# Kernel optimization log

Hardware: AMD Instinct MI355X
Metric: run time of the kernel (lower is better)

The kernel has to match this reference:

```python
import jax, jax.numpy as jnp
import numpy as np
from jax import lax

M_ROWS, N_COLS = 2048, 4096
ADMM_ITERS = 30
CG_ITERS = 15


def setup_inputs() -> dict:
    key = jax.random.key(0)
    ks = jax.random.split(key, 6)
    A = jax.random.normal(ks[0], (M_ROWS, N_COLS), dtype=jnp.float32) / np.sqrt(N_COLS)
    c = jax.random.normal(ks[1], (N_COLS, 1), dtype=jnp.float32)
    # finite box bounds with lb < ub (isinf mask path in the original is vacuous here)
    lb = -(jnp.abs(jax.random.normal(ks[2], (M_ROWS, 1), dtype=jnp.float32)) + 0.1)
    ub = jnp.abs(jax.random.normal(ks[3], (M_ROWS, 1), dtype=jnp.float32)) + 0.1
    # positive diagonal scalings from the LP preconditioning (Ruiz-style)
    d = 0.5 + jax.random.uniform(ks[4], (N_COLS, 1), dtype=jnp.float32)
    e = 0.5 + jax.random.uniform(ks[5], (M_ROWS, 1), dtype=jnp.float32)
    return {
        "A": A, "c": c, "lb": lb, "ub": ub, "d": d, "e": e,
        "gamma_c": jnp.ones((1,), jnp.float32),   # gamma_c_mul * gamma_c
        "gamma_b": jnp.ones((1,), jnp.float32),   # gamma_b_mul * gamma_b
        "rho": jnp.ones((1,), jnp.float32),
        "sigma": jnp.full((1,), 1e-6, jnp.float32),  # exp(sigma_log), sigma_log=log(1e-6)
        "alpha": jnp.full((1,), 1.6, jnp.float32),
    }


def _pcg(matvec, b, Minv, x0, iters):
    """Fixed-iteration preconditioned conjugate gradient for SPD matvec."""
    r0 = b - matvec(x0)
    z0 = Minv(r0)
    rz0 = jnp.vdot(r0, z0)

    def body(carry, _):
        x, r, p, rz = carry
        Kp = matvec(p)
        a = rz / jnp.vdot(p, Kp)
        x = x + a * p
        r = r - a * Kp
        zv = Minv(r)
        rz_new = jnp.vdot(r, zv)
        p = zv + (rz_new / rz) * p
        return (x, r, p, rz_new), None

    (x, _, _, _), _ = lax.scan(body, (x0, r0, z0, rz0), None, length=iters)
    return x


def _admm_lp(A, c, lb, ub, d, e, gamma_c, gamma_b, rho, sigma, alpha):
    gc, gb = gamma_c[0], gamma_b[0]
    rho_s, sig_s, al_s = rho[0], sigma[0], alpha[0]
    m, n = A.shape

    c_s = gc * (d * c)                 # (n,1) scaled cost
    lb_s = gb * e * lb                 # (m,1)
    ub_s = gb * e * ub                 # (m,1)

    # diagonal preconditioner M = sigma + rho * ||A_:,j||^2
    Acnorm2 = jnp.sum(A * A, axis=0)[:, None]      # (n,1)
    Mdiag = sig_s + rho_s * Acnorm2
    Minv = lambda v: v / Mdiag
    Kop = lambda v: rho_s * (A.T @ (A @ v)) + sig_s * v

    x0 = jnp.zeros((n, 1), A.dtype)
    z0 = jnp.zeros((m, 1), A.dtype)
    y0 = jnp.zeros((m, 1), A.dtype)
    xt0 = jnp.zeros((n, 1), A.dtype)

    def step(carry, _):
        x, z, y, xtilde = carry
        right = sig_s * x - c_s + A.T @ (rho_s * z - y)
        xtilde = _pcg(Kop, right, Minv, xtilde, CG_ITERS)
        ztilde = A @ xtilde
        x = al_s * xtilde + (1.0 - al_s) * x
        ztilde = al_s * ztilde + (1.0 - al_s) * z
        z = jnp.clip(ztilde + y / rho_s, lb_s, ub_s)
        y = y + rho_s * (ztilde - z)
        return (x, z, y, xtilde), None

    (x, z, y, xtilde), _ = lax.scan(step, (x0, z0, y0, xt0), None, length=ADMM_ITERS)
    return x * d / gb                   # unscaled LP solution (n,1)


def reference(A, c, lb, ub, d, e, gamma_c, gamma_b, rho, sigma, alpha):
    return _admm_lp(A, c, lb, ub, d, e, gamma_c, gamma_b, rho, sigma, alpha)
```

## Files before the change

kernel.cpp:

```cpp
#include <hip/hip_runtime.h>

#define NWG 256
#define NT  512
#define NDIM 4096
#define MROWS 2048
#define N_ADMM 30
#define N_CG 15

typedef unsigned long long ull;
typedef float f32x4 __attribute__((ext_vector_type(4)));

#define SWZC(c) ((c) ^ (((c) >> 3) & 7))

__device__ __forceinline__ float wred64(float v) {
#pragma unroll
  for (int m = 32; m > 0; m >>= 1) v += __shfl_xor(v, m, 64);
  return v;
}
__device__ __forceinline__ void sta32(unsigned* p, unsigned v) {
  __hip_atomic_store(p, v, __ATOMIC_RELAXED, __HIP_MEMORY_SCOPE_AGENT);
}
__device__ __forceinline__ unsigned lda32(const unsigned* p) {
  return __hip_atomic_load(p, __ATOMIC_RELAXED, __HIP_MEMORY_SCOPE_AGENT);
}
__device__ __forceinline__ void staf(float* p, float v) {
  __hip_atomic_store((unsigned*)p, __float_as_uint(v), __ATOMIC_RELAXED,
                     __HIP_MEMORY_SCOPE_AGENT);
}
__device__ __forceinline__ f32x4 ntf4(const float* p) {
  return __builtin_nontemporal_load((const f32x4*)p);
}
__device__ __forceinline__ float ntf(const float* p) {
  return __builtin_nontemporal_load(p);
}

#define WS_KILL 128
#define WS_FLAG 8192
#define WS_NB0  49152
#define WS_NB1  65536
#define WS_U    81920

__global__ __launch_bounds__(NT, 1)
void admm_lp_kernel(const float* __restrict__ A, const float* __restrict__ cvec,
                    const float* __restrict__ lbv, const float* __restrict__ ubv,
                    const float* __restrict__ dvec, const float* __restrict__ evec,
                    const float* __restrict__ gcp, const float* __restrict__ gbp,
                    const float* __restrict__ rhop, const float* __restrict__ sigp,
                    const float* __restrict__ alp,
                    float* __restrict__ out, unsigned char* __restrict__ ws)
{
  const int tid = threadIdx.x;
  const int w = blockIdx.x;
  const int wv = tid >> 6, lane = tid & 63;
  const int j0 = tid * 8;
  const int q  = tid >> 7;
  const int kt = tid & 127;
  const int gg = tid >> 4, gl = tid & 15;

  unsigned* kill  = (unsigned*)(ws + WS_KILL);
  unsigned* flags = (unsigned*)(ws + WS_FLAG);
  float* nb0 = (float*)(ws + WS_NB0);
  float* nb1 = (float*)(ws + WS_NB1);
  float* u_g = (float*)(ws + WS_U);

  __shared__ float s_scal[8];
  __shared__ float dredA[8], dredB[8];
  __shared__ float dred8[8][8];
  __shared__ float sredA[32][16];
  __shared__ float pmat[16][132];
  __shared__ float cs_lds[16], xchunk[16], diag16[16];
  __shared__ float mzb[8], myb[8], mlb[8], mub[8];
  __shared__ int s_dead;
  __shared__ float ldsA[4096];
  __shared__ float ldsB[4096];

  float Greg[4][32];
  float p8[8], r8[8], xt8[8], x8[8], Md8[8];
  unsigned gen = 0;

  auto wait_prod = [&](unsigned G) {
    if (s_dead) return;
    unsigned* fp = &flags[(size_t)(wv * 32 + (lane & 31)) * 16];
    int spin = 0;
    for (;;) {
      unsigned v = lda32(fp);
      if (__all(v >= G)) break;
      __builtin_amdgcn_s_sleep(1);
      if ((++spin & 127) == 0) {
        if (lda32(kill) != 0u || spin > 2000000) {
          s_dead = 1; sta32(kill, 1u); break;
        }
      }
    }
    asm volatile("" ::: "memory");
    __builtin_amdgcn_sched_barrier(0);
  };

  auto publish = [&]() {
    if (wv == 0) {
      asm volatile("s_waitcnt vmcnt(0)" ::: "memory");
      __builtin_amdgcn_sched_barrier(0);
      if (lane == 0 && !s_dead) sta32(&flags[(size_t)w * 16], gen + 1);
    }
    ++gen;
  };

  if (tid == 0) {
    s_scal[0] = sigp[0]; s_scal[1] = rhop[0]; s_scal[2] = alp[0];
    s_scal[3] = gcp[0];  s_scal[4] = gbp[0];
    s_dead = 0;
  }
  __syncthreads();
  const float sig = s_scal[0], rho = s_scal[1], al = s_scal[2];
  const float gc = s_scal[3], gb = s_scal[4];

  if (tid < 8) {
    const int rm = w * 8 + tid;
    mzb[tid] = 0.f; myb[tid] = 0.f;
    const float ee = evec[rm];
    mlb[tid] = gb * ee * lbv[rm];
    mub[tid] = gb * ee * ubv[rm];
  }
  if (tid < 16) {
    const int j = w * 16 + tid;
    cs_lds[tid] = gc * dvec[j] * cvec[j];
  }

#pragma unroll
  for (int rr = 0; rr < 4; ++rr)
#pragma unroll
    for (int cc = 0; cc < 32; ++cc) Greg[rr][cc] = 0.f;

  {
    f32x4 pf0 = ntf4(A + j0), pf1 = ntf4(A + j0 + 4);
    *(f32x4*)&ldsA[SWZC(2 * tid) * 4]     = pf0;
    *(f32x4*)&ldsA[SWZC(2 * tid + 1) * 4] = pf1;
    pf0 = ntf4(A + NDIM + j0); pf1 = ntf4(A + NDIM + j0 + 4);
    __syncthreads();
    float* bc = ldsA;
    float* bn = ldsB;
#pragma unroll 1
    for (int i = 0; i < MROWS; ++i) {
      if (i + 1 < MROWS) {
        *(f32x4*)&bn[SWZC(2 * tid) * 4]     = pf0;
        *(f32x4*)&bn[SWZC(2 * tid + 1) * 4] = pf1;
      }
      if (i + 2 < MROWS) {
        pf0 = ntf4(A + (size_t)(i + 2) * NDIM + j0);
        pf1 = ntf4(A + (size_t)(i + 2) * NDIM + j0 + 4);
      }
      const f32x4 av = *(f32x4*)&bc[SWZC(w * 4 + q) * 4];
#pragma unroll
      for (int c4 = 0; c4 < 8; ++c4) {
        const f32x4 kv = *(f32x4*)&bc[SWZC(kt * 8 + c4) * 4];
#pragma unroll
        for (int e = 0; e < 4; ++e) {
          const float kvv = kv[e];
          const int cc = c4 * 4 + e;
          Greg[0][cc] += av.x * kvv;
          Greg[1][cc] += av.y * kvv;
          Greg[2][cc] += av.z * kvv;
          Greg[3][cc] += av.w * kvv;
        }
      }
      __syncthreads();
      float* t = bc; bc = bn; bn = t;
    }
  }

  if (kt == (w >> 1)) {
#pragma unroll
    for (int rr = 0; rr < 4; ++rr) {
      const int tc = (w & 1) * 16 + q * 4 + rr;
      float dv = 0.f;
#pragma unroll
      for (int cc = 0; cc < 32; ++cc)
        dv = (cc == tc) ? Greg[rr][cc] : dv;
      diag16[q * 4 + rr] = dv;
    }
  }
  __syncthreads();
  if (tid < 16) staf(&nb1[w * 16 + tid], diag16[tid]);
  publish();
  wait_prod(gen);
  {
    const f32x4 d0 = ntf4(&nb1[j0]), d1 = ntf4(&nb1[j0 + 4]);
#pragma unroll
    for (int e = 0; e < 4; ++e) { Md8[e] = sig + rho * d0[e]; Md8[4 + e] = sig + rho * d1[e]; }
  }
#pragma unroll
  for (int e = 0; e < 8; ++e) { xt8[e] = 0.f; x8[e] = 0.f; }

  float rz = 1.f;

#pragma unroll 1
  for (int admm = 0; admm < N_ADMM; ++admm) {
#pragma unroll 1
    for (int cg = 0; cg <= N_CG; ++cg) {
      if (cg == 0) {
        if (admm == 0) {
          const f32x4 dv0 = ntf4(dvec + j0), dv1 = ntf4(dvec + j0 + 4);
          const f32x4 cv0 = ntf4(cvec + j0), cv1 = ntf4(cvec + j0 + 4);
#pragma unroll
          for (int e = 0; e < 4; ++e) {
            r8[e]     = -gc * dv0[e] * cv0[e];
            r8[4 + e] = -gc * dv1[e] * cv1[e];
          }
        } else {
          wait_prod(gen);
          const float* nb = (gen & 1) ? nb1 : nb0;
          const f32x4 a = ntf4(nb + j0), b = ntf4(nb + j0 + 4);
#pragma unroll
          for (int e = 0; e < 4; ++e) { r8[e] = a[e]; r8[4 + e] = b[e]; }
        }
        float z8[8], part = 0.f;
#pragma unroll
        for (int e = 0; e < 8; ++e) { z8[e] = r8[e] / Md8[e]; part += r8[e] * z8[e]; }
        part = wred64(part);
        if (lane == 0) dredA[wv] = part;
        __syncthreads();
        rz = dredA[0] + dredA[1] + dredA[2] + dredA[3]
           + dredA[4] + dredA[5] + dredA[6] + dredA[7];
#pragma unroll
        for (int e = 0; e < 8; ++e) p8[e] = z8[e];
      } else {
        wait_prod(gen);
        const float* nb = (gen & 1) ? nb1 : nb0;
        const f32x4 a = ntf4(nb + j0), b = ntf4(nb + j0 + 4);
        float Kp8[8];
#pragma unroll
        for (int e = 0; e < 4; ++e) { Kp8[e] = a[e]; Kp8[4 + e] = b[e]; }
        float part = 0.f;
#pragma unroll
        for (int e = 0; e < 8; ++e) part += p8[e] * Kp8[e];
        part = wred64(part);
        if (lane == 0) dredA[wv] = part;
        __syncthreads();
        const float pKp = dredA[0] + dredA[1] + dredA[2] + dredA[3]
                        + dredA[4] + dredA[5] + dredA[6] + dredA[7];
        const float alpha = rz / pKp;
#pragma unroll
        for (int e = 0; e < 8; ++e) xt8[e] += alpha * p8[e];
        if (cg < N_CG) {
          float z8[8], pb = 0.f;
#pragma unroll
          for (int e = 0; e < 8; ++e) {
            r8[e] -= alpha * Kp8[e];
            z8[e] = r8[e] / Md8[e];
            pb += r8[e] * z8[e];
          }
          pb = wred64(pb);
          if (lane == 0) dredB[wv] = pb;
          __syncthreads();
          const float rzn = dredB[0] + dredB[1] + dredB[2] + dredB[3]
                          + dredB[4] + dredB[5] + dredB[6] + dredB[7];
          const float beta = rzn / rz;
          rz = rzn;
#pragma unroll
          for (int e = 0; e < 8; ++e) p8[e] = z8[e] + beta * p8[e];
        }
      }
      if (cg < N_CG) {
        {
          f32x4 v0, v1;
#pragma unroll
          for (int e = 0; e < 4; ++e) { v0[e] = p8[e]; v1[e] = p8[4 + e]; }
          *(f32x4*)&ldsA[SWZC(2 * tid) * 4]     = v0;
          *(f32x4*)&ldsA[SWZC(2 * tid + 1) * 4] = v1;
        }
        __syncthreads();
        float u0 = 0.f, u1 = 0.f, u2 = 0.f, u3 = 0.f;
#pragma unroll
        for (int c4 = 0; c4 < 8; ++c4) {
          const f32x4 kv = *(f32x4*)&ldsA[SWZC(kt * 8 + c4) * 4];
#pragma unroll
          for (int e = 0; e < 4; ++e) {
            const float pv = kv[e];
            const int cc = c4 * 4 + e;
            u0 += Greg[0][cc] * pv; u1 += Greg[1][cc] * pv;
            u2 += Greg[2][cc] * pv; u3 += Greg[3][cc] * pv;
          }
        }
        pmat[q * 4 + 0][kt] = u0; pmat[q * 4 + 1][kt] = u1;
        pmat[q * 4 + 2][kt] = u2; pmat[q * 4 + 3][kt] = u3;
        __syncthreads();
        if (tid < 16) {
          float s = 0.f;
#pragma unroll
          for (int c = 0; c < 32; ++c) {
            const f32x4 vv = *(f32x4*)&pmat[tid][c * 4];
            s += vv[0] + vv[1] + vv[2] + vv[3];
          }
          const int jl = w * 16 + tid;
          const float pv = ldsA[SWZC(jl >> 2) * 4 + (jl & 3)];
          float* nbw = ((gen + 1) & 1) ? nb1 : nb0;
          staf(nbw + jl, rho * s + sig * pv);
        }
        publish();
      } else {
        publish();
      }
    }

    if (admm < N_ADMM - 1) {
#pragma unroll
      for (int r = 0; r < 8; ++r) {
        const float* ap = A + (size_t)(w * 8 + r) * NDIM + j0;
        const f32x4 a = ntf4(ap), b = ntf4(ap + 4);
        float s = a[0] * xt8[0] + a[1] * xt8[1] + a[2] * xt8[2] + a[3] * xt8[3]
                + b[0] * xt8[4] + b[1] * xt8[5] + b[2] * xt8[6] + b[3] * xt8[7];
        s = wred64(s);
        if (lane == 0) dred8[wv][r] = s;
      }
      __syncthreads();
      if (tid < 8) {
        float zt = 0.f;
#pragma unroll
        for (int qq = 0; qq < 8; ++qq) zt += dred8[qq][tid];
        zt = al * zt + (1.f - al) * mzb[tid];
        float zn = fminf(fmaxf(zt + myb[tid] / rho, mlb[tid]), mub[tid]);
        const float yn = myb[tid] + rho * (zt - zn);
        mzb[tid] = zn; myb[tid] = yn;
        staf(&u_g[w * 8 + tid], rho * zn - yn);
      }
#pragma unroll
      for (int e = 0; e < 8; ++e) x8[e] = al * xt8[e] + (1.f - al) * x8[e];
      publish();

      wait_prod(gen);
      {
        const f32x4 uv = ntf4(&u_g[tid * 4]);
        *(f32x4*)&ldsB[tid * 4] = uv;
        f32x4 v0, v1;
#pragma unroll
        for (int e = 0; e < 4; ++e) { v0[e] = xt8[e]; v1[e] = xt8[4 + e]; }
        *(f32x4*)&ldsA[SWZC(2 * tid) * 4]     = v0;
        *(f32x4*)&ldsA[SWZC(2 * tid + 1) * 4] = v1;
        if ((tid >> 1) == w) {
          const int b = (tid & 1) * 8;
#pragma unroll
          for (int e = 0; e < 8; ++e) xchunk[b + e] = x8[e];
        }
      }
      __syncthreads();
      {
        float pr = 0.f;
        const float* acp = A + (size_t)(gg * 64) * NDIM + w * 16 + gl;
#pragma unroll 8
        for (int ii = 0; ii < 64; ++ii)
          pr += ntf(acp + (size_t)ii * NDIM) * ldsB[gg * 64 + ii];
        sredA[gg][gl] = pr;
        float u0 = 0.f, u1 = 0.f, u2 = 0.f, u3 = 0.f;
#pragma unroll
        for (int c4 = 0; c4 < 8; ++c4) {
          const f32x4 kv = *(f32x4*)&ldsA[SWZC(kt * 8 + c4) * 4];
#pragma unroll
          for (int e = 0; e < 4; ++e) {
            const float pv = kv[e];
            const int cc = c4 * 4 + e;
            u0 += Greg[0][cc] * pv; u1 += Greg[1][cc] * pv;
            u2 += Greg[2][cc] * pv; u3 += Greg[3][cc] * pv;
          }
        }
        pmat[q * 4 + 0][kt] = u0; pmat[q * 4 + 1][kt] = u1;
        pmat[q * 4 + 2][kt] = u2; pmat[q * 4 + 3][kt] = u3;
      }
      __syncthreads();
      if (tid < 16) {
        float SR = 0.f;
#pragma unroll
        for (int g32 = 0; g32 < 32; ++g32) SR += sredA[g32][tid];
        float gx = 0.f;
#pragma unroll
        for (int c = 0; c < 32; ++c) {
          const f32x4 vv = *(f32x4*)&pmat[tid][c * 4];
          gx += vv[0] + vv[1] + vv[2] + vv[3];
        }
        const int jl = w * 16 + tid;
        const float xtv = ldsA[SWZC(jl >> 2) * 4 + (jl & 3)];
        const float right = sig * xchunk[tid] - cs_lds[tid] + SR;
        const float Kxt = rho * gx + sig * xtv;
        float* nbw = ((gen + 1) & 1) ? nb1 : nb0;
        staf(nbw + jl, right - Kxt);
      }
      publish();
    }
  }

  if ((tid >> 1) == w) {
    const int b = (tid & 1) * 8;
#pragma unroll
    for (int e = 0; e < 8; ++e) {
      const int j = w * 16 + b + e;
      const float xf = al * xt8[e] + (1.f - al) * x8[e];
      out[j] = xf * dvec[j] / gb;
    }
  }
}

extern "C" void kernel_launch(void* const* d_in, const int* in_sizes, int n_in,
                              void* d_out, int out_size, void* d_ws, size_t ws_size,
                              hipStream_t stream) {
  const float* A   = (const float*)d_in[0];
  const float* c   = (const float*)d_in[1];
  const float* lb  = (const float*)d_in[2];
  const float* ub  = (const float*)d_in[3];
  const float* dv  = (const float*)d_in[4];
  const float* ev  = (const float*)d_in[5];
  const float* gc  = (const float*)d_in[6];
  const float* gb  = (const float*)d_in[7];
  const float* rho = (const float*)d_in[8];
  const float* sg  = (const float*)d_in[9];
  const float* al  = (const float*)d_in[10];
  float* out = (float*)d_out;
  unsigned char* ws = (unsigned char*)d_ws;

  (void)hipMemsetAsync(d_ws, 0, 32768, stream);

  admm_lp_kernel<<<dim3(NWG), dim3(NT), 0, stream>>>(
      A, c, lb, ub, dv, ev, gc, gb, rho, sg, al, out, ws);
}
```

Before: 5.585 ms.

## Recurse G*p via G*z plus beta, retile Gram block, use reciprocal preconditioner

```diff
diff --git a/kernel.cpp b/kernel.cpp
--- a/kernel.cpp
+++ b/kernel.cpp
@@ -7,7 +7,6 @@
 #define N_ADMM 30
 #define N_CG 15
 
-typedef unsigned long long ull;
 typedef float f32x4 __attribute__((ext_vector_type(4)));
 
 #define SWZC(c) ((c) ^ (((c) >> 3) & 7))
@@ -53,8 +52,8 @@
   const int w = blockIdx.x;
   const int wv = tid >> 6, lane = tid & 63;
   const int j0 = tid * 8;
-  const int q  = tid >> 7;
-  const int kt = tid & 127;
+  const int h  = tid >> 8;
+  const int ct = tid & 255;
   const int gg = tid >> 4, gl = tid & 15;
 
   unsigned* kill  = (unsigned*)(ws + WS_KILL);
@@ -65,17 +64,18 @@
 
   __shared__ float s_scal[8];
   __shared__ float dredA[8], dredB[8];
+  __shared__ float dredW[8][8];
   __shared__ float dred8[8][8];
   __shared__ float sredA[32][16];
-  __shared__ float pmat[16][132];
   __shared__ float cs_lds[16], xchunk[16], diag16[16];
   __shared__ float mzb[8], myb[8], mlb[8], mub[8];
   __shared__ int s_dead;
   __shared__ float ldsA[4096];
   __shared__ float ldsB[4096];
 
-  float Greg[4][32];
-  float p8[8], r8[8], xt8[8], x8[8], Md8[8];
+  float Greg[8][16];
+  float p8[8], r8[8], xt8[8], x8[8], mdinv8[8];
+  float gpo = 0.f, p16 = 0.f;
   unsigned gen = 0;
 
   auto wait_prod = [&](unsigned G) {
@@ -85,9 +85,9 @@
     for (;;) {
       unsigned v = lda32(fp);
       if (__all(v >= G)) break;
-      __builtin_amdgcn_s_sleep(1);
-      if ((++spin & 127) == 0) {
-        if (lda32(kill) != 0u || spin > 2000000) {
+      if (++spin > 256) __builtin_amdgcn_s_sleep(1);
+      if ((spin & 1023) == 0) {
+        if (lda32(kill) != 0u || spin > 1500000) {
           s_dead = 1; sta32(kill, 1u); break;
         }
       }
@@ -103,6 +103,29 @@
       if (lane == 0 && !s_dead) sta32(&flags[(size_t)w * 16], gen + 1);
     }
     ++gen;
+  };
+
+  auto gmult_stage = [&]() {
+    const f32x4 kv0 = *(const f32x4*)&ldsA[SWZC(ct * 4 + 0) * 4];
+    const f32x4 kv1 = *(const f32x4*)&ldsA[SWZC(ct * 4 + 1) * 4];
+    const f32x4 kv2 = *(const f32x4*)&ldsA[SWZC(ct * 4 + 2) * 4];
+    const f32x4 kv3 = *(const f32x4*)&ldsA[SWZC(ct * 4 + 3) * 4];
+    float u[8];
+#pragma unroll
+    for (int rr = 0; rr < 8; ++rr) {
+      float s = 0.f;
+#pragma unroll
+      for (int e = 0; e < 4; ++e) {
+        s += Greg[rr][e] * kv0[e] + Greg[rr][4 + e] * kv1[e]
+           + Greg[rr][8 + e] * kv2[e] + Greg[rr][12 + e] * kv3[e];
+      }
+      u[rr] = s;
+    }
+#pragma unroll
+    for (int rr = 0; rr < 8; ++rr) {
+      const float t = wred64(u[rr]);
+      if (lane == 0) dredW[wv][rr] = t;
+    }
   };
 
   if (tid == 0) {
@@ -127,9 +150,9 @@
   }
 
 #pragma unroll
-  for (int rr = 0; rr < 4; ++rr)
-#pragma unroll
-    for (int cc = 0; cc < 32; ++cc) Greg[rr][cc] = 0.f;
+  for (int rr = 0; rr < 8; ++rr)
+#pragma unroll
+    for (int c = 0; c < 16; ++c) Greg[rr][c] = 0.f;
 
   {
     f32x4 pf0 = ntf4(A + j0), pf1 = ntf4(A + j0 + 4);
@@ -149,18 +172,24 @@
         pf0 = ntf4(A + (size_t)(i + 2) * NDIM + j0);
         pf1 = ntf4(A + (size_t)(i + 2) * NDIM + j0 + 4);
       }
-      const f32x4 av = *(f32x4*)&bc[SWZC(w * 4 + q) * 4];
-#pragma unroll
-      for (int c4 = 0; c4 < 8; ++c4) {
-        const f32x4 kv = *(f32x4*)&bc[SWZC(kt * 8 + c4) * 4];
+      const f32x4 a0 = *(const f32x4*)&bc[SWZC(w * 4 + h * 2) * 4];
+      const f32x4 a1 = *(const f32x4*)&bc[SWZC(w * 4 + h * 2 + 1) * 4];
+      const f32x4 k0 = *(const f32x4*)&bc[SWZC(ct * 4 + 0) * 4];
+      const f32x4 k1 = *(const f32x4*)&bc[SWZC(ct * 4 + 1) * 4];
+      const f32x4 k2 = *(const f32x4*)&bc[SWZC(ct * 4 + 2) * 4];
+      const f32x4 k3 = *(const f32x4*)&bc[SWZC(ct * 4 + 3) * 4];
+#pragma unroll
+      for (int rr = 0; rr < 4; ++rr) {
 #pragma unroll
         for (int e = 0; e < 4; ++e) {
-          const float kvv = kv[e];
-          const int cc = c4 * 4 + e;
-          Greg[0][cc] += av.x * kvv;
-          Greg[1][cc] += av.y * kvv;
-          Greg[2][cc] += av.z * kvv;
-          Greg[3][cc] += av.w * kvv;
+          Greg[rr][e]      += a0[rr] * k0[e];
+          Greg[rr][4 + e]  += a0[rr] * k1[e];
+          Greg[rr][8 + e]  += a0[rr] * k2[e];
+          Greg[rr][12 + e] += a0[rr] * k3[e];
+          Greg[4 + rr][e]      += a1[rr] * k0[e];
+          Greg[4 + rr][4 + e]  += a1[rr] * k1[e];
+          Greg[4 + rr][8 + e]  += a1[rr] * k2[e];
+          Greg[4 + rr][12 + e] += a1[rr] * k3[e];
         }
       }
       __syncthreads();
@@ -168,15 +197,13 @@
     }
   }
 
-  if (kt == (w >> 1)) {
-#pragma unroll
-    for (int rr = 0; rr < 4; ++rr) {
-      const int tc = (w & 1) * 16 + q * 4 + rr;
-      float dv = 0.f;
-#pragma unroll
-      for (int cc = 0; cc < 32; ++cc)
-        dv = (cc == tc) ? Greg[rr][cc] : dv;
-      diag16[q * 4 + rr] = dv;
+  if (ct == w) {
+    if (h == 0) {
+#pragma unroll
+      for (int rr = 0; rr < 8; ++rr) diag16[rr] = Greg[rr][rr];
+    } else {
+#pragma unroll
+      for (int rr = 0; rr < 8; ++rr) diag16[8 + rr] = Greg[rr][8 + rr];
     }
   }
   __syncthreads();
@@ -186,7 +213,10 @@
   {
     const f32x4 d0 = ntf4(&nb1[j0]), d1 = ntf4(&nb1[j0 + 4]);
 #pragma unroll
-    for (int e = 0; e < 4; ++e) { Md8[e] = sig + rho * d0[e]; Md8[4 + e] = sig + rho * d1[e]; }
+    for (int e = 0; e < 4; ++e) {
+      mdinv8[e]     = 1.f / (sig + rho * d0[e]);
+      mdinv8[4 + e] = 1.f / (sig + rho * d1[e]);
+    }
   }
 #pragma unroll
   for (int e = 0; e < 8; ++e) { xt8[e] = 0.f; x8[e] = 0.f; }
@@ -213,16 +243,36 @@
 #pragma unroll
           for (int e = 0; e < 4; ++e) { r8[e] = a[e]; r8[4 + e] = b[e]; }
         }
-        float z8[8], part = 0.f;
-#pragma unroll
-        for (int e = 0; e < 8; ++e) { z8[e] = r8[e] / Md8[e]; part += r8[e] * z8[e]; }
-        part = wred64(part);
-        if (lane == 0) dredA[wv] = part;
+        float z8[8], pb = 0.f;
+#pragma unroll
+        for (int e = 0; e < 8; ++e) { z8[e] = r8[e] * mdinv8[e]; pb += r8[e] * z8[e]; }
+        {
+          f32x4 v0, v1;
+#pragma unroll
+          for (int e = 0; e < 4; ++e) { v0[e] = z8[e]; v1[e] = z8[4 + e]; }
+          *(f32x4*)&ldsA[SWZC(2 * tid) * 4]     = v0;
+          *(f32x4*)&ldsA[SWZC(2 * tid + 1) * 4] = v1;
+        }
+        pb = wred64(pb);
+        if (lane == 0) dredB[wv] = pb;
         __syncthreads();
-        rz = dredA[0] + dredA[1] + dredA[2] + dredA[3]
-           + dredA[4] + dredA[5] + dredA[6] + dredA[7];
+        rz = dredB[0] + dredB[1] + dredB[2] + dredB[3]
+           + dredB[4] + dredB[5] + dredB[6] + dredB[7];
 #pragma unroll
         for (int e = 0; e < 8; ++e) p8[e] = z8[e];
+        gmult_stage();
+        __syncthreads();
+        if (tid < 16) {
+          const int h2 = tid >> 3, rr = tid & 7;
+          const float gz = dredW[h2 * 4 + 0][rr] + dredW[h2 * 4 + 1][rr]
+                         + dredW[h2 * 4 + 2][rr] + dredW[h2 * 4 + 3][rr];
+          gpo = gz;
+          const int idx = w * 16 + tid;
+          p16 = ldsA[SWZC(idx >> 2) * 4 + (idx & 3)];
+          float* nbw = ((gen + 1) & 1) ? nb1 : nb0;
+          staf(nbw + idx, rho * gz + sig * p16);
+        }
+        publish();
       } else {
         wait_prod(gen);
         const float* nb = (gen & 1) ? nb1 : nb0;
@@ -246,8 +296,15 @@
 #pragma unroll
           for (int e = 0; e < 8; ++e) {
             r8[e] -= alpha * Kp8[e];
-            z8[e] = r8[e] / Md8[e];
+            z8[e] = r8[e] * mdinv8[e];
             pb += r8[e] * z8[e];
+          }
+          {
+            f32x4 v0, v1;
+#pragma unroll
+            for (int e = 0; e < 4; ++e) { v0[e] = z8[e]; v1[e] = z8[4 + e]; }
+            *(f32x4*)&ldsA[SWZC(2 * tid) * 4]     = v0;
+            *(f32x4*)&ldsA[SWZC(2 * tid + 1) * 4] = v1;
           }
           pb = wred64(pb);
           if (lane == 0) dredB[wv] = pb;
@@ -258,47 +315,24 @@
           rz = rzn;
 #pragma unroll
           for (int e = 0; e < 8; ++e) p8[e] = z8[e] + beta * p8[e];
-        }
-      }
-      if (cg < N_CG) {
-        {
-          f32x4 v0, v1;
-#pragma unroll
-          for (int e = 0; e < 4; ++e) { v0[e] = p8[e]; v1[e] = p8[4 + e]; }
-          *(f32x4*)&ldsA[SWZC(2 * tid) * 4]     = v0;
-          *(f32x4*)&ldsA[SWZC(2 * tid + 1) * 4] = v1;
-        }
-        __syncthreads();
-        float u0 = 0.f, u1 = 0.f, u2 = 0.f, u3 = 0.f;
-#pragma unroll
-        for (int c4 = 0; c4 < 8; ++c4) {
-          const f32x4 kv = *(f32x4*)&ldsA[SWZC(kt * 8 + c4) * 4];
-#pragma unroll
-          for (int e = 0; e < 4; ++e) {
-            const float pv = kv[e];
-            const int cc = c4 * 4 + e;
-            u0 += Greg[0][cc] * pv; u1 += Greg[1][cc] * pv;
-            u2 += Greg[2][cc] * pv; u3 += Greg[3][cc] * pv;
+          gmult_stage();
+          __syncthreads();
+          if (tid < 16) {
+            const int h2 = tid >> 3, rr = tid & 7;
+            const float gz = dredW[h2 * 4 + 0][rr] + dredW[h2 * 4 + 1][rr]
+                           + dredW[h2 * 4 + 2][rr] + dredW[h2 * 4 + 3][rr];
+            const float gp = gz + beta * gpo;
+            gpo = gp;
+            const int idx = w * 16 + tid;
+            const float z16 = ldsA[SWZC(idx >> 2) * 4 + (idx & 3)];
+            p16 = z16 + beta * p16;
+            float* nbw = ((gen + 1) & 1) ? nb1 : nb0;
+            staf(nbw + idx, rho * gp + sig * p16);
           }
-        }
-        pmat[q * 4 + 0][kt] = u0; pmat[q * 4 + 1][kt] = u1;
-        pmat[q * 4 + 2][kt] = u2; pmat[q * 4 + 3][kt] = u3;
-        __syncthreads();
-        if (tid < 16) {
-          float s = 0.f;
-#pragma unroll
-          for (int c = 0; c < 32; ++c) {
-            const f32x4 vv = *(f32x4*)&pmat[tid][c * 4];
-            s += vv[0] + vv[1] + vv[2] + vv[3];
-          }
-          const int jl = w * 16 + tid;
-          const float pv = ldsA[SWZC(jl >> 2) * 4 + (jl & 3)];
-          float* nbw = ((gen + 1) & 1) ? nb1 : nb0;
-          staf(nbw + jl, rho * s + sig * pv);
-        }
-        publish();
-      } else {
-        publish();
+          publish();
+        } else {
+          publish();
+        }
       }
     }
 
@@ -350,38 +384,22 @@
         for (int ii = 0; ii < 64; ++ii)
           pr += ntf(acp + (size_t)ii * NDIM) * ldsB[gg * 64 + ii];
         sredA[gg][gl] = pr;
-        float u0 = 0.f, u1 = 0.f, u2 = 0.f, u3 = 0.f;
-#pragma unroll
-        for (int c4 = 0; c4 < 8; ++c4) {
-          const f32x4 kv = *(f32x4*)&ldsA[SWZC(kt * 8 + c4) * 4];
-#pragma unroll
-          for (int e = 0; e < 4; ++e) {
-            const float pv = kv[e];
-            const int cc = c4 * 4 + e;
-            u0 += Greg[0][cc] * pv; u1 += Greg[1][cc] * pv;
-            u2 += Greg[2][cc] * pv; u3 += Greg[3][cc] * pv;
-          }
-        }
-        pmat[q * 4 + 0][kt] = u0; pmat[q * 4 + 1][kt] = u1;
-        pmat[q * 4 + 2][kt] = u2; pmat[q * 4 + 3][kt] = u3;
+        gmult_stage();
       }
       __syncthreads();
       if (tid < 16) {
         float SR = 0.f;
 #pragma unroll
         for (int g32 = 0; g32 < 32; ++g32) SR += sredA[g32][tid];
-        float gx = 0.f;
-#pragma unroll
-        for (int c = 0; c < 32; ++c) {
-          const f32x4 vv = *(f32x4*)&pmat[tid][c * 4];
-          gx += vv[0] + vv[1] + vv[2] + vv[3];
-        }
-        const int jl = w * 16 + tid;
-        const float xtv = ldsA[SWZC(jl >> 2) * 4 + (jl & 3)];
+        const int h2 = tid >> 3, rr = tid & 7;
+        const float gxt = dredW[h2 * 4 + 0][rr] + dredW[h2 * 4 + 1][rr]
+                        + dredW[h2 * 4 + 2][rr] + dredW[h2 * 4 + 3][rr];
+        const int idx = w * 16 + tid;
+        const float xtv = ldsA[SWZC(idx >> 2) * 4 + (idx & 3)];
         const float right = sig * xchunk[tid] - cs_lds[tid] + SR;
-        const float Kxt = rho * gx + sig * xtv;
+        const float Kxt = rho * gxt + sig * xtv;
         float* nbw = ((gen + 1) & 1) ? nb1 : nb0;
-        staf(nbw + jl, right - Kxt);
+        staf(nbw + idx, right - Kxt);
       }
       publish();
     }
```

New measurement: 5.888 ms. 1.05x slower.
